# Performance work log

Measured on AMD Instinct MI355X. Metric: run time of the kernel, lower is better.

## Reference

```python
import jax, jax.numpy as jnp
import numpy as np

B, N, D, O = 16384, 784, 8, 10   # batch, num_sites, bond_dim, output_dim
LABEL = N // 2                   # 392
L_LEFT = LABEL - 1               # sites 1..391 -> 391 mid tensors
L_RIGHT = N - 2 - LABEL          # sites 393..782 -> 390 mid tensors


def setup_inputs() -> dict:
    key = jax.random.key(0)
    k0, k1, k2, k3, k4, k5 = jax.random.split(key, 6)
    x = jax.random.uniform(k0, (B, N, 1), dtype=jnp.float32)
    # scale mid tensors so the 784-site matrix product stays O(1):
    # per-site variance multiplier ~ D * var(w) * E[phi^2]*2 with E[phi^2]=1/3
    s_mid = (3.0 / (2.0 * D)) ** 0.5
    w0 = jax.random.normal(k1, (2, D), dtype=jnp.float32) * 1.2
    W_left = jax.random.normal(k2, (L_LEFT, D, 2, D), dtype=jnp.float32) * s_mid
    w_label = jax.random.normal(k3, (D, 2, D, O), dtype=jnp.float32) * s_mid
    W_right = jax.random.normal(k4, (L_RIGHT, D, 2, D), dtype=jnp.float32) * s_mid
    w_last = jax.random.normal(k5, (D, 2), dtype=jnp.float32) * 1.2
    return {"x": x, "w0": w0, "W_left": W_left, "w_label": w_label,
            "W_right": W_right, "w_last": w_last}


def reference(x, w0, W_left, w_label, W_right, w_last):
    p = jnp.squeeze(x, axis=-1)                       # [B, N]
    phi = jnp.stack([1.0 - p, p], axis=-1)            # [B, N, 2] feature map

    # site 0: [B,2] x [2,D] -> left boundary vector [B,D]
    v = jnp.einsum('bf,fd->bd', phi[:, 0], w0)

    def step_left(v, xw):
        phi_i, w_i = xw                               # [B,2], [D,2,D]
        return jnp.einsum('bd,dfe,bf->be', v, w_i, phi_i), None

    phiL = jnp.transpose(phi[:, 1:LABEL], (1, 0, 2))  # [L_LEFT, B, 2]
    v, _ = jax.lax.scan(step_left, v, (phiL, W_left))

    # label site: [B,D] x [D,2,D,O] x [B,2] -> [B,D,O]
    v = jnp.einsum('bd,dfeo,bf->beo', v, w_label, phi[:, LABEL])

    def step_right(v, xw):
        phi_i, w_i = xw
        return jnp.einsum('bdo,dfe,bf->beo', v, w_i, phi_i), None

    phiR = jnp.transpose(phi[:, LABEL + 1:N - 1], (1, 0, 2))  # [L_RIGHT, B, 2]
    v, _ = jax.lax.scan(step_right, v, (phiR, W_right))

    # last site: right boundary vector [B,D], then close the chain -> [B,O]
    r = jnp.einsum('bf,df->bd', phi[:, N - 1], w_last)
    return jnp.einsum('bdo,bd->bo', v, r)
```

## Files before the change

kernel.cpp:

```cpp
#include <hip/hip_runtime.h>


#define NSITES 784
#define DIM    8
#define ODIM   10
#define LABEL  392
#define WSITE  144
#define QST    36
#define XST    20

typedef float v2f __attribute__((ext_vector_type(2)));

__device__ __forceinline__ float dpp_q1(float s){float d;asm("v_mov_b32_dpp %0, %1 quad_perm:[1,0,3,2] row_mask:0xf bank_mask:0xf":"=v"(d):"v"(s));return d;}
__device__ __forceinline__ float dpp_q2(float s){float d;asm("v_mov_b32_dpp %0, %1 quad_perm:[2,3,0,1] row_mask:0xf bank_mask:0xf":"=v"(d):"v"(s));return d;}
__device__ __forceinline__ float dpp_q3(float s){float d;asm("v_mov_b32_dpp %0, %1 quad_perm:[3,2,1,0] row_mask:0xf bank_mask:0xf":"=v"(d):"v"(s));return d;}

__device__ __forceinline__ v2f pk_mul(v2f a, v2f b){v2f d;asm("v_pk_mul_f32 %0,%1,%2":"=v"(d):"v"(a),"v"(b));return d;}
__device__ __forceinline__ v2f pk_fma(v2f a, v2f b, v2f c){v2f d;asm("v_pk_fma_f32 %0,%1,%2,%3":"=v"(d):"v"(a),"v"(b),"v"(c));return d;}
__device__ __forceinline__ v2f pk_fma_s(v2f a, v2f b, v2f c){v2f d;asm("v_pk_fma_f32 %0,%1,%2,%3 op_sel:[1,0,0] op_sel_hi:[0,1,1]":"=v"(d):"v"(a),"v"(b),"v"(c));return d;}
__device__ __forceinline__ v2f pk_fma_blo(v2f a, v2f b, v2f c){v2f d;asm("v_pk_fma_f32 %0,%1,%2,%3 op_sel:[0,0,0] op_sel_hi:[0,1,1]":"=v"(d):"v"(a),"v"(b),"v"(c));return d;}
__device__ __forceinline__ v2f pk_fma_bhi(v2f a, v2f b, v2f c){v2f d;asm("v_pk_fma_f32 %0,%1,%2,%3 op_sel:[1,0,0] op_sel_hi:[1,1,1]":"=v"(d):"v"(a),"v"(b),"v"(c));return d;}
__device__ __forceinline__ v2f pk_sub(v2f a, v2f b){v2f d;asm("v_pk_add_f32 %0,%1,%2 neg_lo:[0,1] neg_hi:[0,1]":"=v"(d):"v"(a),"v"(b));return d;}

__device__ __forceinline__ v2f XY(const float4& q){ v2f r = {q.x, q.y}; return r; }
__device__ __forceinline__ v2f ZW(const float4& q){ v2f r = {q.z, q.w}; return r; }

template <bool PHI>
__device__ __forceinline__ v2f site_step(v2f v, const float* wc, v2f pp) {
    const float4 r0 = *(const float4*)(wc + 0);
    const float4 r1 = *(const float4*)(wc + 4);
    const float4 r2 = *(const float4*)(wc + 8);
    const float4 r3 = *(const float4*)(wc + 12);
    const float4 r4 = *(const float4*)(wc + 16);
    const float4 r5 = *(const float4*)(wc + 20);
    const float4 r6 = *(const float4*)(wc + 24);
    const float4 r7 = *(const float4*)(wc + 28);
    v2f d1; d1.x = dpp_q1(v.x); d1.y = dpp_q1(v.y);
    v2f d2; d2.x = dpp_q2(v.x); d2.y = dpp_q2(v.y);
    v2f d3; d3.x = dpp_q3(v.x); d3.y = dpp_q3(v.y);
    v2f a0 = pk_mul (v,  XY(r0));
    a0 = pk_fma_s(v,  ZW(r0), a0);
    a0 = pk_fma  (d1, XY(r1), a0);
    a0 = pk_fma_s(d1, ZW(r1), a0);
    a0 = pk_fma  (d2, XY(r2), a0);
    a0 = pk_fma_s(d2, ZW(r2), a0);
    a0 = pk_fma  (d3, XY(r3), a0);
    a0 = pk_fma_s(d3, ZW(r3), a0);
    v2f a1 = pk_mul (v,  XY(r4));
    a1 = pk_fma_s(v,  ZW(r4), a1);
    a1 = pk_fma  (d1, XY(r5), a1);
    a1 = pk_fma_s(d1, ZW(r5), a1);
    a1 = pk_fma  (d2, XY(r6), a1);
    a1 = pk_fma_s(d2, ZW(r6), a1);
    a1 = pk_fma  (d3, XY(r7), a1);
    a1 = pk_fma_s(d3, ZW(r7), a1);
    const v2f df = pk_sub(a1, a0);
    return PHI ? pk_fma_bhi(pp, df, a0) : pk_fma_blo(pp, df, a0);
}

__global__ __launch_bounds__(256, 2) void mps_fused(
    const float* __restrict__ x,
    const float* __restrict__ w0,
    const float* __restrict__ Wl,
    const float* __restrict__ wlab,
    const float* __restrict__ Wr,
    const float* __restrict__ wlast,
    float* __restrict__ out)
{
    __shared__ float wb[2][2][16 * WSITE];
    __shared__ float xb[2][2][32 * XST];
    __shared__ float wl[1280];
    __shared__ float vout[2][256];

    const int tid  = threadIdx.x;
    const int side = tid >> 7;
    const int stid = tid & 127;
    const int w    = stid >> 6;
    const int lane = stid & 63;
    const int q    = lane & 3;
    const int grp  = lane >> 2;
    const int bl   = w * 16 + grp;
    const int b0   = blockIdx.x * 32;

    for (int k = tid; k < 320; k += 256)
        *(float4*)&wl[k * 4] = *(const float4*)&wlab[k * 4];

    float4 wr[4];
    float  xr[4];

    auto stage_load = [&](int c, int nt) {
        const float* W = side == 0 ? Wl : Wr;
        #pragma unroll
        for (int r = 0; r < 4; ++r) {
            const int cid = stid + 128 * r;
            const int s   = cid >> 5;
            const int u   = cid & 31;
            if (s < nt) {
                const int row = side == 0 ? (c * 16 + s) : (389 - c * 16 - s);
                wr[r] = *(const float4*)(W + (size_t)row * 128 + u * 4);
            }
        }
        #pragma unroll
        for (int r = 0; r < 4; ++r) {
            const int cid = stid + 128 * r;
            const int b   = cid >> 4;
            const int sx  = cid & 15;
            if (sx < nt) {
                const int col = side == 0 ? (1 + c * 16 + sx) : (782 - c * 16 - sx);
                xr[r] = x[(size_t)(b0 + b) * NSITES + col];
            }
        }
    };

    auto stage_write = [&](int bufi, int nt) {
        float* wdst = wb[side][bufi];
        float* xdst = xb[side][bufi];
        #pragma unroll
        for (int r = 0; r < 4; ++r) {
            const int cid = stid + 128 * r;
            const int s   = cid >> 5;
            const int u   = cid & 31;
            const int d   = u >> 2;
            const int f   = (u >> 1) & 1;
            const int e4  = (u & 1) * 4;
            if (s < nt) {
                float* dst = wdst + s * WSITE;
                const float vals[4] = {wr[r].x, wr[r].y, wr[r].z, wr[r].w};
                #pragma unroll
                for (int k = 0; k < 4; ++k) {
                    const int e = e4 + k;
                    if (side == 0)
                        dst[(e >> 1) * QST + (f * 8 + (e ^ d)) * 2 + (e & 1)] = vals[k];
                    else
                        dst[(d >> 1) * QST + (f * 8 + (d ^ e)) * 2 + (d & 1)] = vals[k];
                }
            }
        }
        #pragma unroll
        for (int r = 0; r < 4; ++r) {
            const int cid = stid + 128 * r;
            const int b   = cid >> 4;
            const int sx  = cid & 15;
            if (sx < nt)
                xdst[b * XST + sx] = xr[r];
        }
    };

    v2f vv;
    {
        const int e0 = 2 * q, e1 = 2 * q + 1;
        if (side == 0) {
            const float p = x[(size_t)(b0 + bl) * NSITES];
            vv.x = fmaf(1.0f - p, w0[e0], p * w0[DIM + e0]);
            vv.y = fmaf(1.0f - p, w0[e1], p * w0[DIM + e1]);
        } else {
            const float p = x[(size_t)(b0 + bl) * NSITES + (NSITES - 1)];
            vv.x = fmaf(1.0f - p, wlast[e0 * 2], p * wlast[e0 * 2 + 1]);
            vv.y = fmaf(1.0f - p, wlast[e1 * 2], p * wlast[e1 * 2 + 1]);
        }
    }

    const int nt_tail = side ? 6 : 7;

    stage_load(0, 16);
    stage_write(0, 16);
    int buf = 0;

    auto compute16 = [&](int bufi) {
        const float* wp = &wb[side][bufi][q * QST];
        const float* xp = &xb[side][bufi][bl * XST];
        #pragma unroll
        for (int jb = 0; jb < 4; ++jb) {
            const float4 xq = *(const float4*)(xp + jb * 4);
            const v2f p01 = XY(xq);
            const v2f p23 = ZW(xq);
            vv = site_step<false>(vv, wp + (jb * 4 + 0) * WSITE, p01);
            vv = site_step<true >(vv, wp + (jb * 4 + 1) * WSITE, p01);
            vv = site_step<false>(vv, wp + (jb * 4 + 2) * WSITE, p23);
            vv = site_step<true >(vv, wp + (jb * 4 + 3) * WSITE, p23);
        }
    };

    #pragma unroll 1
    for (int c = 0; c < 23; ++c) {
        __syncthreads();
        stage_load(c + 1, 16);
        compute16(buf);
        __builtin_amdgcn_sched_barrier(0);
        stage_write(buf ^ 1, 16);
        buf ^= 1;
    }

    __syncthreads();
    stage_load(24, nt_tail);
    compute16(buf);
    __builtin_amdgcn_sched_barrier(0);
    stage_write(buf ^ 1, nt_tail);
    buf ^= 1;

    __syncthreads();
    {
        const float* wp = &wb[side][buf][q * QST];
        const float* xp = &xb[side][buf][bl * XST];
        for (int j = 0; j < nt_tail; ++j) {
            v2f pp; pp.x = xp[j]; pp.y = pp.x;
            vv = site_step<false>(vv, wp + j * WSITE, pp);
        }
    }

    *(v2f*)&vout[side][bl * 8 + 2 * q] = vv;
    __syncthreads();

    for (int idx = tid; idx < 320; idx += 256) {
        const int b = idx / 10;
        const int o = idx - b * 10;
        const float p = x[(size_t)(b0 + b) * NSITES + LABEL];
        const float qq = 1.0f - p;
        const float* vl = &vout[0][b * 8];
        const float* rv = &vout[1][b * 8];
        float acc = 0.0f;
        #pragma unroll
        for (int d = 0; d < DIM; ++d) {
            const float vld = vl[d];
            #pragma unroll
            for (int ee = 0; ee < DIM; ++ee) {
                const float m = fmaf(qq, wl[((d * 2 + 0) * DIM + ee) * ODIM + o],
                                     p * wl[((d * 2 + 1) * DIM + ee) * ODIM + o]);
                acc = fmaf(vld * rv[ee], m, acc);
            }
        }
        out[(size_t)(b0 + b) * ODIM + o] = acc;
    }
}

extern "C" void kernel_launch(void* const* d_in, const int* in_sizes, int n_in,
                              void* d_out, int out_size, void* d_ws, size_t ws_size,
                              hipStream_t stream) {
    (void)in_sizes; (void)n_in; (void)d_ws; (void)ws_size; (void)out_size;
    const float* x     = (const float*)d_in[0];
    const float* w0    = (const float*)d_in[1];
    const float* Wl    = (const float*)d_in[2];
    const float* wlab  = (const float*)d_in[3];
    const float* Wr    = (const float*)d_in[4];
    const float* wlast = (const float*)d_in[5];

    mps_fused<<<512, 256, 0, stream>>>(x, w0, Wl, wlab, Wr, wlast, (float*)d_out);
}
```

Baseline: 154.0 us.

## Process two batch rows per thread and software-pipeline weight LDS loads

Halves the block to 128 threads (one wave per chain side), with each thread now carrying two independent boundary vectors (batch rows g and g+16). Each site's weight fragment is read from LDS once into registers and reused for both rows, and the next site's weights are prefetched into a double-buffered register set. This is meant to halve LDS weight traffic per flop and give two independent dependency chains for ILP. In exchange there are fewer waves per CU and more register pressure, and the global staging loads per thread double.

```diff
diff --git a/kernel.cpp b/kernel.cpp
--- a/kernel.cpp
+++ b/kernel.cpp
@@ -26,39 +26,31 @@
 __device__ __forceinline__ v2f ZW(const float4& q){ v2f r = {q.z, q.w}; return r; }
 
 template <bool PHI>
-__device__ __forceinline__ v2f site_step(v2f v, const float* wc, v2f pp) {
-    const float4 r0 = *(const float4*)(wc + 0);
-    const float4 r1 = *(const float4*)(wc + 4);
-    const float4 r2 = *(const float4*)(wc + 8);
-    const float4 r3 = *(const float4*)(wc + 12);
-    const float4 r4 = *(const float4*)(wc + 16);
-    const float4 r5 = *(const float4*)(wc + 20);
-    const float4 r6 = *(const float4*)(wc + 24);
-    const float4 r7 = *(const float4*)(wc + 28);
+__device__ __forceinline__ v2f site_step(v2f v, const float4 (&r)[8], v2f pp) {
     v2f d1; d1.x = dpp_q1(v.x); d1.y = dpp_q1(v.y);
     v2f d2; d2.x = dpp_q2(v.x); d2.y = dpp_q2(v.y);
     v2f d3; d3.x = dpp_q3(v.x); d3.y = dpp_q3(v.y);
-    v2f a0 = pk_mul (v,  XY(r0));
-    a0 = pk_fma_s(v,  ZW(r0), a0);
-    a0 = pk_fma  (d1, XY(r1), a0);
-    a0 = pk_fma_s(d1, ZW(r1), a0);
-    a0 = pk_fma  (d2, XY(r2), a0);
-    a0 = pk_fma_s(d2, ZW(r2), a0);
-    a0 = pk_fma  (d3, XY(r3), a0);
-    a0 = pk_fma_s(d3, ZW(r3), a0);
-    v2f a1 = pk_mul (v,  XY(r4));
-    a1 = pk_fma_s(v,  ZW(r4), a1);
-    a1 = pk_fma  (d1, XY(r5), a1);
-    a1 = pk_fma_s(d1, ZW(r5), a1);
-    a1 = pk_fma  (d2, XY(r6), a1);
-    a1 = pk_fma_s(d2, ZW(r6), a1);
-    a1 = pk_fma  (d3, XY(r7), a1);
-    a1 = pk_fma_s(d3, ZW(r7), a1);
+    v2f a0 = pk_mul (v,  XY(r[0]));
+    a0 = pk_fma_s(v,  ZW(r[0]), a0);
+    a0 = pk_fma  (d1, XY(r[1]), a0);
+    a0 = pk_fma_s(d1, ZW(r[1]), a0);
+    a0 = pk_fma  (d2, XY(r[2]), a0);
+    a0 = pk_fma_s(d2, ZW(r[2]), a0);
+    a0 = pk_fma  (d3, XY(r[3]), a0);
+    a0 = pk_fma_s(d3, ZW(r[3]), a0);
+    v2f a1 = pk_mul (v,  XY(r[4]));
+    a1 = pk_fma_s(v,  ZW(r[4]), a1);
+    a1 = pk_fma  (d1, XY(r[5]), a1);
+    a1 = pk_fma_s(d1, ZW(r[5]), a1);
+    a1 = pk_fma  (d2, XY(r[6]), a1);
+    a1 = pk_fma_s(d2, ZW(r[6]), a1);
+    a1 = pk_fma  (d3, XY(r[7]), a1);
+    a1 = pk_fma_s(d3, ZW(r[7]), a1);
     const v2f df = pk_sub(a1, a0);
     return PHI ? pk_fma_bhi(pp, df, a0) : pk_fma_blo(pp, df, a0);
 }
 
-__global__ __launch_bounds__(256, 2) void mps_fused(
+__global__ __launch_bounds__(128, 1) void mps_fused(
     const float* __restrict__ x,
     const float* __restrict__ w0,
     const float* __restrict__ Wl,
@@ -73,26 +65,25 @@
     __shared__ float vout[2][256];
 
     const int tid  = threadIdx.x;
-    const int side = tid >> 7;
-    const int stid = tid & 127;
-    const int w    = stid >> 6;
-    const int lane = stid & 63;
-    const int q    = lane & 3;
-    const int grp  = lane >> 2;
-    const int bl   = w * 16 + grp;
+    const int side = tid >> 6;
+    const int stid = tid & 63;
+    const int q    = stid & 3;
+    const int g    = stid >> 2;
+    const int bl0  = g;
+    const int bl1  = g + 16;
     const int b0   = blockIdx.x * 32;
 
-    for (int k = tid; k < 320; k += 256)
+    for (int k = tid; k < 320; k += 128)
         *(float4*)&wl[k * 4] = *(const float4*)&wlab[k * 4];
 
-    float4 wr[4];
-    float  xr[4];
+    float4 wr[8];
+    float  xr[8];
 
     auto stage_load = [&](int c, int nt) {
         const float* W = side == 0 ? Wl : Wr;
         #pragma unroll
-        for (int r = 0; r < 4; ++r) {
-            const int cid = stid + 128 * r;
+        for (int r = 0; r < 8; ++r) {
+            const int cid = stid + 64 * r;
             const int s   = cid >> 5;
             const int u   = cid & 31;
             if (s < nt) {
@@ -101,8 +92,8 @@
             }
         }
         #pragma unroll
-        for (int r = 0; r < 4; ++r) {
-            const int cid = stid + 128 * r;
+        for (int r = 0; r < 8; ++r) {
+            const int cid = stid + 64 * r;
             const int b   = cid >> 4;
             const int sx  = cid & 15;
             if (sx < nt) {
@@ -116,8 +107,8 @@
         float* wdst = wb[side][bufi];
         float* xdst = xb[side][bufi];
         #pragma unroll
-        for (int r = 0; r < 4; ++r) {
-            const int cid = stid + 128 * r;
+        for (int r = 0; r < 8; ++r) {
+            const int cid = stid + 64 * r;
             const int s   = cid >> 5;
             const int u   = cid & 31;
             const int d   = u >> 2;
@@ -137,8 +128,8 @@
             }
         }
         #pragma unroll
-        for (int r = 0; r < 4; ++r) {
-            const int cid = stid + 128 * r;
+        for (int r = 0; r < 8; ++r) {
+            const int cid = stid + 64 * r;
             const int b   = cid >> 4;
             const int sx  = cid & 15;
             if (sx < nt)
@@ -146,17 +137,23 @@
         }
     };
 
-    v2f vv;
+    v2f vv0, vv1;
     {
         const int e0 = 2 * q, e1 = 2 * q + 1;
         if (side == 0) {
-            const float p = x[(size_t)(b0 + bl) * NSITES];
-            vv.x = fmaf(1.0f - p, w0[e0], p * w0[DIM + e0]);
-            vv.y = fmaf(1.0f - p, w0[e1], p * w0[DIM + e1]);
+            const float p0 = x[(size_t)(b0 + bl0) * NSITES];
+            const float p1 = x[(size_t)(b0 + bl1) * NSITES];
+            vv0.x = fmaf(1.0f - p0, w0[e0], p0 * w0[DIM + e0]);
+            vv0.y = fmaf(1.0f - p0, w0[e1], p0 * w0[DIM + e1]);
+            vv1.x = fmaf(1.0f - p1, w0[e0], p1 * w0[DIM + e0]);
+            vv1.y = fmaf(1.0f - p1, w0[e1], p1 * w0[DIM + e1]);
         } else {
-            const float p = x[(size_t)(b0 + bl) * NSITES + (NSITES - 1)];
-            vv.x = fmaf(1.0f - p, wlast[e0 * 2], p * wlast[e0 * 2 + 1]);
-            vv.y = fmaf(1.0f - p, wlast[e1 * 2], p * wlast[e1 * 2 + 1]);
+            const float p0 = x[(size_t)(b0 + bl0) * NSITES + (NSITES - 1)];
+            const float p1 = x[(size_t)(b0 + bl1) * NSITES + (NSITES - 1)];
+            vv0.x = fmaf(1.0f - p0, wlast[e0 * 2], p0 * wlast[e0 * 2 + 1]);
+            vv0.y = fmaf(1.0f - p0, wlast[e1 * 2], p0 * wlast[e1 * 2 + 1]);
+            vv1.x = fmaf(1.0f - p1, wlast[e0 * 2], p1 * wlast[e0 * 2 + 1]);
+            vv1.y = fmaf(1.0f - p1, wlast[e1 * 2], p1 * wlast[e1 * 2 + 1]);
         }
     }
 
@@ -167,17 +164,34 @@
     int buf = 0;
 
     auto compute16 = [&](int bufi) {
-        const float* wp = &wb[side][bufi][q * QST];
-        const float* xp = &xb[side][bufi][bl * XST];
-        #pragma unroll
-        for (int jb = 0; jb < 4; ++jb) {
-            const float4 xq = *(const float4*)(xp + jb * 4);
-            const v2f p01 = XY(xq);
-            const v2f p23 = ZW(xq);
-            vv = site_step<false>(vv, wp + (jb * 4 + 0) * WSITE, p01);
-            vv = site_step<true >(vv, wp + (jb * 4 + 1) * WSITE, p01);
-            vv = site_step<false>(vv, wp + (jb * 4 + 2) * WSITE, p23);
-            vv = site_step<true >(vv, wp + (jb * 4 + 3) * WSITE, p23);
+        const float* wp  = &wb[side][bufi][q * QST];
+        const float* xp0 = &xb[side][bufi][bl0 * XST];
+        const float* xp1 = &xb[side][bufi][bl1 * XST];
+        float4 wg[2][8];
+        #pragma unroll
+        for (int i = 0; i < 8; ++i)
+            wg[0][i] = *(const float4*)(wp + i * 4);
+        float4 xqA, xqB;
+        #pragma unroll
+        for (int j = 0; j < 16; ++j) {
+            if ((j & 3) == 0) {
+                xqA = *(const float4*)(xp0 + j);
+                xqB = *(const float4*)(xp1 + j);
+            }
+            if (j < 15) {
+                #pragma unroll
+                for (int i = 0; i < 8; ++i)
+                    wg[(j + 1) & 1][i] = *(const float4*)(wp + (j + 1) * WSITE + i * 4);
+            }
+            const v2f pA = (j & 2) ? ZW(xqA) : XY(xqA);
+            const v2f pB = (j & 2) ? ZW(xqB) : XY(xqB);
+            if (j & 1) {
+                vv0 = site_step<true >(vv0, wg[j & 1], pA);
+                vv1 = site_step<true >(vv1, wg[j & 1], pB);
+            } else {
+                vv0 = site_step<false>(vv0, wg[j & 1], pA);
+                vv1 = site_step<false>(vv1, wg[j & 1], pB);
+            }
         }
     };
 
@@ -200,18 +214,26 @@
 
     __syncthreads();
     {
-        const float* wp = &wb[side][buf][q * QST];
-        const float* xp = &xb[side][buf][bl * XST];
+        const float* wp  = &wb[side][buf][q * QST];
+        const float* xp0 = &xb[side][buf][bl0 * XST];
+        const float* xp1 = &xb[side][buf][bl1 * XST];
         for (int j = 0; j < nt_tail; ++j) {
-            v2f pp; pp.x = xp[j]; pp.y = pp.x;
-            vv = site_step<false>(vv, wp + j * WSITE, pp);
-        }
-    }
-
-    *(v2f*)&vout[side][bl * 8 + 2 * q] = vv;
+            float4 r[8];
+            #pragma unroll
+            for (int i = 0; i < 8; ++i)
+                r[i] = *(const float4*)(wp + j * WSITE + i * 4);
+            v2f pA; pA.x = xp0[j]; pA.y = pA.x;
+            v2f pB; pB.x = xp1[j]; pB.y = pB.x;
+            vv0 = site_step<false>(vv0, r, pA);
+            vv1 = site_step<false>(vv1, r, pB);
+        }
+    }
+
+    *(v2f*)&vout[side][bl0 * 8 + 2 * q] = vv0;
+    *(v2f*)&vout[side][bl1 * 8 + 2 * q] = vv1;
     __syncthreads();
 
-    for (int idx = tid; idx < 320; idx += 256) {
+    for (int idx = tid; idx < 320; idx += 128) {
         const int b = idx / 10;
         const int o = idx - b * 10;
         const float p = x[(size_t)(b0 + b) * NSITES + LABEL];
@@ -244,5 +266,5 @@
     const float* Wr    = (const float*)d_in[4];
     const float* wlast = (const float*)d_in[5];
 
-    mps_fused<<<512, 256, 0, stream>>>(x, w0, Wl, wlab, Wr, wlast, (float*)d_out);
+    mps_fused<<<512, 128, 0, stream>>>(x, w0, Wl, wlab, Wr, wlast, (float*)d_out);
 }
```

Result: slower. 191.0 us (+24.0%).

## Remap threads to one bond index per lane, two batch rows per lane

Applied to the files above, without the earlier changes.

Changes the work split from 4 lanes holding 2 bond components each for one sample to 8 lanes holding one bond component each for two samples, packed into v2f. The per-site step now reads 16 weight floats instead of 32 from LDS, and the weights are broadcast across both samples using op_sel. In exchange it needs 7 DPP shuffles per component instead of 3 (including a half-row mirror), and the LDS weight and x layouts are rewritten to match. The aim is to cut LDS read traffic and weight-register pressure per FMA.

```diff
diff --git a/kernel.cpp b/kernel.cpp
--- a/kernel.cpp
+++ b/kernel.cpp
@@ -5,57 +5,56 @@
 #define DIM    8
 #define ODIM   10
 #define LABEL  392
-#define WSITE  144
-#define QST    36
-#define XST    20
+#define WSITE  160
+#define CST    20
+#define XPST   34
 
 typedef float v2f __attribute__((ext_vector_type(2)));
 
 __device__ __forceinline__ float dpp_q1(float s){float d;asm("v_mov_b32_dpp %0, %1 quad_perm:[1,0,3,2] row_mask:0xf bank_mask:0xf":"=v"(d):"v"(s));return d;}
 __device__ __forceinline__ float dpp_q2(float s){float d;asm("v_mov_b32_dpp %0, %1 quad_perm:[2,3,0,1] row_mask:0xf bank_mask:0xf":"=v"(d):"v"(s));return d;}
 __device__ __forceinline__ float dpp_q3(float s){float d;asm("v_mov_b32_dpp %0, %1 quad_perm:[3,2,1,0] row_mask:0xf bank_mask:0xf":"=v"(d):"v"(s));return d;}
-
-__device__ __forceinline__ v2f pk_mul(v2f a, v2f b){v2f d;asm("v_pk_mul_f32 %0,%1,%2":"=v"(d):"v"(a),"v"(b));return d;}
+__device__ __forceinline__ float dpp_x7(float s){float d;asm("v_mov_b32_dpp %0, %1 row_half_mirror row_mask:0xf bank_mask:0xf":"=v"(d):"v"(s));return d;}
+
 __device__ __forceinline__ v2f pk_fma(v2f a, v2f b, v2f c){v2f d;asm("v_pk_fma_f32 %0,%1,%2,%3":"=v"(d):"v"(a),"v"(b),"v"(c));return d;}
-__device__ __forceinline__ v2f pk_fma_s(v2f a, v2f b, v2f c){v2f d;asm("v_pk_fma_f32 %0,%1,%2,%3 op_sel:[1,0,0] op_sel_hi:[0,1,1]":"=v"(d):"v"(a),"v"(b),"v"(c));return d;}
-__device__ __forceinline__ v2f pk_fma_blo(v2f a, v2f b, v2f c){v2f d;asm("v_pk_fma_f32 %0,%1,%2,%3 op_sel:[0,0,0] op_sel_hi:[0,1,1]":"=v"(d):"v"(a),"v"(b),"v"(c));return d;}
-__device__ __forceinline__ v2f pk_fma_bhi(v2f a, v2f b, v2f c){v2f d;asm("v_pk_fma_f32 %0,%1,%2,%3 op_sel:[1,0,0] op_sel_hi:[1,1,1]":"=v"(d):"v"(a),"v"(b),"v"(c));return d;}
 __device__ __forceinline__ v2f pk_sub(v2f a, v2f b){v2f d;asm("v_pk_add_f32 %0,%1,%2 neg_lo:[0,1] neg_hi:[0,1]":"=v"(d):"v"(a),"v"(b));return d;}
+__device__ __forceinline__ v2f pk_mul_blo(v2f a, v2f b){v2f d;asm("v_pk_mul_f32 %0,%1,%2 op_sel:[0,0] op_sel_hi:[1,0]":"=v"(d):"v"(a),"v"(b));return d;}
+__device__ __forceinline__ v2f pk_fma_blo(v2f a, v2f b, v2f c){v2f d;asm("v_pk_fma_f32 %0,%1,%2,%3 op_sel:[0,0,0] op_sel_hi:[1,0,1]":"=v"(d):"v"(a),"v"(b),"v"(c));return d;}
+__device__ __forceinline__ v2f pk_fma_bhi(v2f a, v2f b, v2f c){v2f d;asm("v_pk_fma_f32 %0,%1,%2,%3 op_sel:[0,1,0] op_sel_hi:[1,1,1]":"=v"(d):"v"(a),"v"(b),"v"(c));return d;}
 
 __device__ __forceinline__ v2f XY(const float4& q){ v2f r = {q.x, q.y}; return r; }
 __device__ __forceinline__ v2f ZW(const float4& q){ v2f r = {q.z, q.w}; return r; }
 
-template <bool PHI>
 __device__ __forceinline__ v2f site_step(v2f v, const float* wc, v2f pp) {
     const float4 r0 = *(const float4*)(wc + 0);
     const float4 r1 = *(const float4*)(wc + 4);
     const float4 r2 = *(const float4*)(wc + 8);
     const float4 r3 = *(const float4*)(wc + 12);
-    const float4 r4 = *(const float4*)(wc + 16);
-    const float4 r5 = *(const float4*)(wc + 20);
-    const float4 r6 = *(const float4*)(wc + 24);
-    const float4 r7 = *(const float4*)(wc + 28);
-    v2f d1; d1.x = dpp_q1(v.x); d1.y = dpp_q1(v.y);
-    v2f d2; d2.x = dpp_q2(v.x); d2.y = dpp_q2(v.y);
-    v2f d3; d3.x = dpp_q3(v.x); d3.y = dpp_q3(v.y);
-    v2f a0 = pk_mul (v,  XY(r0));
-    a0 = pk_fma_s(v,  ZW(r0), a0);
-    a0 = pk_fma  (d1, XY(r1), a0);
-    a0 = pk_fma_s(d1, ZW(r1), a0);
-    a0 = pk_fma  (d2, XY(r2), a0);
-    a0 = pk_fma_s(d2, ZW(r2), a0);
-    a0 = pk_fma  (d3, XY(r3), a0);
-    a0 = pk_fma_s(d3, ZW(r3), a0);
-    v2f a1 = pk_mul (v,  XY(r4));
-    a1 = pk_fma_s(v,  ZW(r4), a1);
-    a1 = pk_fma  (d1, XY(r5), a1);
-    a1 = pk_fma_s(d1, ZW(r5), a1);
-    a1 = pk_fma  (d2, XY(r6), a1);
-    a1 = pk_fma_s(d2, ZW(r6), a1);
-    a1 = pk_fma  (d3, XY(r7), a1);
-    a1 = pk_fma_s(d3, ZW(r7), a1);
+    v2f t1; t1.x = dpp_q1(v.x);  t1.y = dpp_q1(v.y);
+    v2f t2; t2.x = dpp_q2(v.x);  t2.y = dpp_q2(v.y);
+    v2f t3; t3.x = dpp_q3(v.x);  t3.y = dpp_q3(v.y);
+    v2f t7; t7.x = dpp_x7(v.x);  t7.y = dpp_x7(v.y);
+    v2f t6; t6.x = dpp_q1(t7.x); t6.y = dpp_q1(t7.y);
+    v2f t5; t5.x = dpp_q2(t7.x); t5.y = dpp_q2(t7.y);
+    v2f t4; t4.x = dpp_q3(t7.x); t4.y = dpp_q3(t7.y);
+    v2f a0 = pk_mul_blo(v,  XY(r0));
+    a0 = pk_fma_bhi(t1, XY(r0), a0);
+    a0 = pk_fma_blo(t2, ZW(r0), a0);
+    a0 = pk_fma_bhi(t3, ZW(r0), a0);
+    a0 = pk_fma_blo(t4, XY(r1), a0);
+    a0 = pk_fma_bhi(t5, XY(r1), a0);
+    a0 = pk_fma_blo(t6, ZW(r1), a0);
+    a0 = pk_fma_bhi(t7, ZW(r1), a0);
+    v2f a1 = pk_mul_blo(v,  XY(r2));
+    a1 = pk_fma_bhi(t1, XY(r2), a1);
+    a1 = pk_fma_blo(t2, ZW(r2), a1);
+    a1 = pk_fma_bhi(t3, ZW(r2), a1);
+    a1 = pk_fma_blo(t4, XY(r3), a1);
+    a1 = pk_fma_bhi(t5, XY(r3), a1);
+    a1 = pk_fma_blo(t6, ZW(r3), a1);
+    a1 = pk_fma_bhi(t7, ZW(r3), a1);
     const v2f df = pk_sub(a1, a0);
-    return PHI ? pk_fma_bhi(pp, df, a0) : pk_fma_blo(pp, df, a0);
+    return pk_fma(pp, df, a0);
 }
 
 __global__ __launch_bounds__(256, 2) void mps_fused(
@@ -68,7 +67,7 @@
     float* __restrict__ out)
 {
     __shared__ float wb[2][2][16 * WSITE];
-    __shared__ float xb[2][2][32 * XST];
+    __shared__ float xb[2][2][16 * XPST];
     __shared__ float wl[1280];
     __shared__ float vout[2][256];
 
@@ -77,9 +76,11 @@
     const int stid = tid & 127;
     const int w    = stid >> 6;
     const int lane = stid & 63;
-    const int q    = lane & 3;
-    const int grp  = lane >> 2;
-    const int bl   = w * 16 + grp;
+    const int e    = lane & 7;
+    const int g    = lane >> 3;
+    const int pr   = w * 8 + g;
+    const int bl0  = w * 16 + g;
+    const int bl1  = w * 16 + 8 + g;
     const int b0   = blockIdx.x * 32;
 
     for (int k = tid; k < 320; k += 256)
@@ -124,40 +125,41 @@
             const int f   = (u >> 1) & 1;
             const int e4  = (u & 1) * 4;
             if (s < nt) {
-                float* dst = wdst + s * WSITE;
+                float* dst = wdst + s * WSITE + f * 8;
                 const float vals[4] = {wr[r].x, wr[r].y, wr[r].z, wr[r].w};
                 #pragma unroll
                 for (int k = 0; k < 4; ++k) {
-                    const int e = e4 + k;
+                    const int ee = e4 + k;
                     if (side == 0)
-                        dst[(e >> 1) * QST + (f * 8 + (e ^ d)) * 2 + (e & 1)] = vals[k];
+                        dst[ee * CST + (ee ^ d)] = vals[k];
                     else
-                        dst[(d >> 1) * QST + (f * 8 + (d ^ e)) * 2 + (d & 1)] = vals[k];
+                        dst[d * CST + (d ^ ee)] = vals[k];
                 }
             }
         }
         #pragma unroll
         for (int r = 0; r < 4; ++r) {
-            const int cid = stid + 128 * r;
-            const int b   = cid >> 4;
-            const int sx  = cid & 15;
+            const int cid  = stid + 128 * r;
+            const int b    = cid >> 4;
+            const int sx   = cid & 15;
+            const int prw  = (b >> 4) * 8 + (b & 7);
+            const int half = (b >> 3) & 1;
             if (sx < nt)
-                xdst[b * XST + sx] = xr[r];
+                xdst[prw * XPST + sx * 2 + half] = xr[r];
         }
     };
 
     v2f vv;
-    {
-        const int e0 = 2 * q, e1 = 2 * q + 1;
-        if (side == 0) {
-            const float p = x[(size_t)(b0 + bl) * NSITES];
-            vv.x = fmaf(1.0f - p, w0[e0], p * w0[DIM + e0]);
-            vv.y = fmaf(1.0f - p, w0[e1], p * w0[DIM + e1]);
-        } else {
-            const float p = x[(size_t)(b0 + bl) * NSITES + (NSITES - 1)];
-            vv.x = fmaf(1.0f - p, wlast[e0 * 2], p * wlast[e0 * 2 + 1]);
-            vv.y = fmaf(1.0f - p, wlast[e1 * 2], p * wlast[e1 * 2 + 1]);
-        }
+    if (side == 0) {
+        const float p0 = x[(size_t)(b0 + bl0) * NSITES];
+        const float p1 = x[(size_t)(b0 + bl1) * NSITES];
+        vv.x = fmaf(1.0f - p0, w0[e], p0 * w0[DIM + e]);
+        vv.y = fmaf(1.0f - p1, w0[e], p1 * w0[DIM + e]);
+    } else {
+        const float p0 = x[(size_t)(b0 + bl0) * NSITES + (NSITES - 1)];
+        const float p1 = x[(size_t)(b0 + bl1) * NSITES + (NSITES - 1)];
+        vv.x = fmaf(1.0f - p0, wlast[e * 2], p0 * wlast[e * 2 + 1]);
+        vv.y = fmaf(1.0f - p1, wlast[e * 2], p1 * wlast[e * 2 + 1]);
     }
 
     const int nt_tail = side ? 6 : 7;
@@ -167,17 +169,13 @@
     int buf = 0;
 
     auto compute16 = [&](int bufi) {
-        const float* wp = &wb[side][bufi][q * QST];
-        const float* xp = &xb[side][bufi][bl * XST];
-        #pragma unroll
-        for (int jb = 0; jb < 4; ++jb) {
-            const float4 xq = *(const float4*)(xp + jb * 4);
-            const v2f p01 = XY(xq);
-            const v2f p23 = ZW(xq);
-            vv = site_step<false>(vv, wp + (jb * 4 + 0) * WSITE, p01);
-            vv = site_step<true >(vv, wp + (jb * 4 + 1) * WSITE, p01);
-            vv = site_step<false>(vv, wp + (jb * 4 + 2) * WSITE, p23);
-            vv = site_step<true >(vv, wp + (jb * 4 + 3) * WSITE, p23);
+        const float* wp = &wb[side][bufi][e * CST];
+        const float* xp = &xb[side][bufi][pr * XPST];
+        #pragma unroll
+        for (int jh = 0; jh < 8; ++jh) {
+            const float4 xq = *(const float4*)(xp + jh * 4);
+            vv = site_step(vv, wp + (2 * jh + 0) * WSITE, XY(xq));
+            vv = site_step(vv, wp + (2 * jh + 1) * WSITE, ZW(xq));
         }
     };
 
@@ -200,15 +198,16 @@
 
     __syncthreads();
     {
-        const float* wp = &wb[side][buf][q * QST];
-        const float* xp = &xb[side][buf][bl * XST];
+        const float* wp = &wb[side][buf][e * CST];
+        const float* xp = &xb[side][buf][pr * XPST];
         for (int j = 0; j < nt_tail; ++j) {
-            v2f pp; pp.x = xp[j]; pp.y = pp.x;
-            vv = site_step<false>(vv, wp + j * WSITE, pp);
-        }
-    }
-
-    *(v2f*)&vout[side][bl * 8 + 2 * q] = vv;
+            v2f pp; pp.x = xp[j * 2]; pp.y = xp[j * 2 + 1];
+            vv = site_step(vv, wp + j * WSITE, pp);
+        }
+    }
+
+    vout[side][bl0 * 8 + e] = vv.x;
+    vout[side][bl1 * 8 + e] = vv.y;
     __syncthreads();
 
     for (int idx = tid; idx < 320; idx += 256) {
```

New measurement: 181.9 us. 18.1% more time.
